# Kernel optimization log

Measured on AMD Instinct MI355X. Metric: run time of the kernel, lower is better.

## Reference

```python
import jax, jax.numpy as jnp
import numpy as np

H = 16
D_MODEL = 1024
D_K = D_MODEL // H
L = 4096


def setup_inputs() -> dict:
    key = jax.random.key(0)
    ks = jax.random.split(key, 11)
    s = 1.0 / np.sqrt(D_MODEL)
    inp = {
        "query": jax.random.normal(ks[0], (L, D_MODEL), dtype=jnp.float32),
        "key": jax.random.normal(ks[1], (L, D_MODEL), dtype=jnp.float32),
        "value": jax.random.normal(ks[2], (L, D_MODEL), dtype=jnp.float32),
        "Wq": jax.random.uniform(ks[3], (D_MODEL, D_MODEL), jnp.float32, -s, s),
        "Wk": jax.random.uniform(ks[4], (D_MODEL, D_MODEL), jnp.float32, -s, s),
        "Wv": jax.random.uniform(ks[5], (D_MODEL, D_MODEL), jnp.float32, -s, s),
        "Wo": jax.random.uniform(ks[6], (D_MODEL, D_MODEL), jnp.float32, -s, s),
        "bq": jax.random.uniform(ks[7], (D_MODEL,), jnp.float32, -s, s),
        "bk": jax.random.uniform(ks[8], (D_MODEL,), jnp.float32, -s, s),
        "bv": jax.random.uniform(ks[9], (D_MODEL,), jnp.float32, -s, s),
        "bo": jax.random.uniform(ks[10], (D_MODEL,), jnp.float32, -s, s),
    }
    return inp


def reference(query, key, value, Wq, Wk, Wv, Wo, bq, bk, bv, bo):
    # projections: torch Linear computes x @ W.T + b
    def proj(x, W, b):
        # [L, d_model] -> [h, L, d_k]
        y = x @ W.T + b
        return y.reshape(L, H, D_K).transpose(1, 0, 2)

    q = proj(query, Wq, bq)   # [h, L, d_k]
    k = proj(key, Wk, bk)
    v = proj(value, Wv, bv)

    scores = jnp.einsum("hqd,hkd->hqk", q, k) / jnp.sqrt(jnp.float32(D_K))  # [h, L, L]
    p = jax.nn.softmax(scores, axis=-1)
    x = jnp.einsum("hqk,hkd->hqd", p, v)         # [h, L, d_k]
    x = x.transpose(1, 0, 2).reshape(L, H * D_K)  # [L, d_model]
    return x @ Wo.T + bo
```

## Files before the change

### kernel.cpp

```cpp
#include <hip/hip_runtime.h>

#define L_SEQ 4096
#define DM 1024
#define NH 16
#define DK 64

typedef short s16x8 __attribute__((ext_vector_type(8)));
typedef float f32x4 __attribute__((ext_vector_type(4)));
typedef float f32x8 __attribute__((ext_vector_type(8)));
typedef float f32x16 __attribute__((ext_vector_type(16)));
typedef unsigned short u16t;
typedef unsigned int u32t;

typedef __attribute__((address_space(1))) unsigned int as1_u32;
typedef __attribute__((address_space(3))) unsigned int as3_u32;

#define GLOAD_LDS16(gsrc, ldst) \
  __builtin_amdgcn_global_load_lds((as1_u32*)(gsrc), (as3_u32*)(ldst), 16, 0, 0)

__device__ __forceinline__ u16t f2bf(float f) {
  union { float f; unsigned u; } v; v.f = f;
  unsigned u = v.u;
  u += 0x7fffu + ((u >> 16) & 1u);
  return (u16t)(u >> 16);
}

__device__ __forceinline__ float fexp2(float x) {
  float r;
  asm("v_exp_f32 %0, %1" : "=v"(r) : "v"(x));
  return r;
}

__device__ __forceinline__ float bflo(u32t u) {
  union { u32t u; float f; } v; v.u = u << 16; return v.f;
}
__device__ __forceinline__ float bfhi(u32t u) {
  union { u32t u; float f; } v; v.u = u & 0xffff0000u; return v.f;
}

struct CvtArgs { const float* s[7]; u16t* d[7]; };

__global__ __launch_bounds__(256) void cvt_all(CvtArgs a) {
  int g = blockIdx.x * 256 + threadIdx.x;
  int seg, off;
  if (g < 1572864) { seg = g >> 19;               off = g & 524287; }
  else             { int t = g - 1572864; seg = 3 + (t >> 17); off = t & 131071; }
  const float* src = a.s[seg] + (size_t)off * 8;
  u16t* dst = a.d[seg] + (size_t)off * 8;
  float4 x = *(const float4*)(src);
  float4 y = *(const float4*)(src + 4);
  uint4 o;
  o.x = (u32t)f2bf(x.x) | ((u32t)f2bf(x.y) << 16);
  o.y = (u32t)f2bf(x.z) | ((u32t)f2bf(x.w) << 16);
  o.z = (u32t)f2bf(y.x) | ((u32t)f2bf(y.y) << 16);
  o.w = (u32t)f2bf(y.z) | ((u32t)f2bf(y.w) << 16);
  *(uint4*)dst = o;
}

struct QkvArgs {
  const u16t* A[3]; const u16t* Bm[3]; const float* bias[3]; u16t* C[3];
  float scale0;
};

__global__ __launch_bounds__(256)
void gemm_qkv(QkvArgs ga) {
  __shared__ unsigned char lds[2][2][8192];
  const int flat = blockIdx.x;
  const int bid = (flat & 7) * 96 + (flat >> 3);
  const int z = bid >> 8;
  const int b = bid & 255;
  const int bc = (z == 2) ? (b & 31) : (b & 7);
  const int br = (z == 2) ? (b >> 5) : (b >> 3);
  const int N  = (z == 2) ? L_SEQ : DM;
  const float osc = (z == 0) ? ga.scale0 : 1.0f;
  const bool rowb = (z == 2);
  const u16t* A = ga.A[z];
  const u16t* Bm = ga.Bm[z];
  const float* bias = ga.bias[z];
  u16t* C = ga.C[z];
  const int K = DM;

  const int tid = threadIdx.x;
  const int lane = tid & 63;
  const int wv = tid >> 6;
  const int wr = wv >> 1, wc = wv & 1;
  const int l15 = lane & 15, l4 = lane >> 4;

  const int r_st = tid >> 2;
  const int c_st = (tid & 3) ^ ((r_st >> 1) & 3);
  const u16t* a0 = A + (size_t)(br * 128 + r_st) * K + c_st * 8;
  const u16t* a1 = a0 + (size_t)64 * K;
  const u16t* b0 = Bm + (size_t)(bc * 128 + r_st) * K + c_st * 8;
  const u16t* b1 = b0 + (size_t)64 * K;
  const int woff = wv * 1024;

  f32x4 acc[4][4] = {};

  auto stage = [&](int buf, int k0) {
    GLOAD_LDS16(a0 + k0, &lds[buf][0][woff]);
    GLOAD_LDS16(a1 + k0, &lds[buf][0][4096 + woff]);
    GLOAD_LDS16(b0 + k0, &lds[buf][1][woff]);
    GLOAD_LDS16(b1 + k0, &lds[buf][1][4096 + woff]);
  };

  const int nt = K >> 5;
  stage(0, 0);
  int buf = 0;
  for (int t = 0; t < nt; ++t) {
    __syncthreads();
    if (t + 1 < nt) stage(buf ^ 1, (t + 1) * 32);
    s16x8 af[4], bfr[4];
    #pragma unroll
    for (int m = 0; m < 4; ++m) {
      int r = wr * 64 + m * 16 + l15;
      int sl = l4 ^ ((r >> 1) & 3);
      af[m] = *(const s16x8*)&lds[buf][0][r * 64 + (sl << 4)];
    }
    #pragma unroll
    for (int n = 0; n < 4; ++n) {
      int r = wc * 64 + n * 16 + l15;
      int sl = l4 ^ ((r >> 1) & 3);
      bfr[n] = *(const s16x8*)&lds[buf][1][r * 64 + (sl << 4)];
    }
    #pragma unroll
    for (int m = 0; m < 4; ++m)
      #pragma unroll
      for (int n = 0; n < 4; ++n)
        acc[m][n] = __builtin_amdgcn_mfma_f32_16x16x32_bf16(af[m], bfr[n], acc[m][n], 0, 0, 0);
    buf ^= 1;
  }

  const int l15p = rowb ? ((l15 & 3) | ((l15 & 4) << 1) | ((l15 & 8) >> 1)) : l15;

  #pragma unroll
  for (int m = 0; m < 4; ++m) {
    #pragma unroll
    for (int n = 0; n < 4; ++n) {
      #pragma unroll
      for (int i = 0; i < 4; ++i) {
        int row = br * 128 + wr * 64 + m * 16 + l4 * 4 + i;
        int col = bc * 128 + wc * 64 + n * 16 + l15p;
        float v = (acc[m][n][i] + (rowb ? bias[row] : bias[col])) * osc;
        C[(size_t)row * N + col] = f2bf(v);
      }
    }
  }
}

__global__ __launch_bounds__(256)
void gemm_out(const u16t* __restrict__ A, const u16t* __restrict__ B,
              const float* __restrict__ bias, float* __restrict__ C,
              int M, int N, int K) {
  __shared__ unsigned char lds[2][12288];
  const int tid = threadIdx.x;
  const int lane = tid & 63;
  const int wv = tid >> 6;
  const int wr = wv >> 1, wc = wv & 1;
  const int l15 = lane & 15, l4 = lane >> 4;
  const int flat = blockIdx.x + (blockIdx.y << 4);
  const int nsw = (flat & 7) * 64 + (flat >> 3);
  const int bc = nsw & 15, br = nsw >> 4;

  const int r_st = tid >> 2;
  const int c_st = (tid & 3) ^ ((r_st >> 1) & 3);
  const u16t* a0 = A + (size_t)(br * 128 + r_st) * K + c_st * 8;
  const u16t* a1 = a0 + (size_t)64 * K;
  const u16t* b0 = B + (size_t)(bc * 64 + r_st) * K + c_st * 8;
  const int woff = wv * 1024;

  f32x4 acc[4][2] = {};

  auto stage = [&](int buf, int k0) {
    GLOAD_LDS16(a0 + k0, &lds[buf][woff]);
    GLOAD_LDS16(a1 + k0, &lds[buf][4096 + woff]);
    GLOAD_LDS16(b0 + k0, &lds[buf][8192 + woff]);
  };

  const int nt = K >> 5;
  stage(0, 0);
  int buf = 0;
  for (int t = 0; t < nt; ++t) {
    __syncthreads();
    if (t + 1 < nt) stage(buf ^ 1, (t + 1) * 32);
    s16x8 af[4], bfr[2];
    #pragma unroll
    for (int m = 0; m < 4; ++m) {
      int r = wr * 64 + m * 16 + l15;
      int sl = l4 ^ ((r >> 1) & 3);
      af[m] = *(const s16x8*)&lds[buf][r * 64 + (sl << 4)];
    }
    #pragma unroll
    for (int n = 0; n < 2; ++n) {
      int r = wc * 32 + n * 16 + l15;
      int sl = l4 ^ ((r >> 1) & 3);
      bfr[n] = *(const s16x8*)&lds[buf][8192 + r * 64 + (sl << 4)];
    }
    #pragma unroll
    for (int m = 0; m < 4; ++m)
      #pragma unroll
      for (int n = 0; n < 2; ++n)
        acc[m][n] = __builtin_amdgcn_mfma_f32_16x16x32_bf16(af[m], bfr[n], acc[m][n], 0, 0, 0);
    buf ^= 1;
  }

  #pragma unroll
  for (int m = 0; m < 4; ++m) {
    #pragma unroll
    for (int n = 0; n < 2; ++n) {
      #pragma unroll
      for (int i = 0; i < 4; ++i) {
        int row = br * 128 + wr * 64 + m * 16 + l4 * 4 + i;
        int col = bc * 64 + wc * 32 + n * 16 + l15;
        C[(size_t)row * N + col] = acc[m][n][i] + bias[col];
      }
    }
  }
}

#define PKBF(dst, a, b) \
  asm("v_cvt_pk_bf16_f32 %0, %1, %2" : "=v"(dst) : "v"(a), "v"(b))

#define MAKE_FRAG(S, B, FR) { \
    union { u32t u[4]; s16x8 v; } uu; \
    PKBF(uu.u[0], S[B + 0], S[B + 1]); \
    PKBF(uu.u[1], S[B + 2], S[B + 3]); \
    PKBF(uu.u[2], S[B + 4], S[B + 5]); \
    PKBF(uu.u[3], S[B + 6], S[B + 7]); \
    FR = uu.v; }

__global__ __launch_bounds__(512, 4)
void attn_fused(const u16t* __restrict__ Qp, const u16t* __restrict__ Kp,
                const u16t* __restrict__ VpT, u16t* __restrict__ Op,
                float* __restrict__ Ml) {
  __shared__ unsigned char sStage[3][16384];

  const int tid = threadIdx.x;
  const int lane = tid & 63;
  const int w = tid >> 6;
  const int l31 = lane & 31;
  const int hi = lane >> 5;
  const int flat = blockIdx.x;
  const int nsw = (flat & 7) * 64 + (flat >> 3);
  const int qt = nsw & 15;
  const int h = (nsw >> 4) & 15;
  const int z = nsw >> 8;
  const int kvbase = z * (L_SEQ / 2);
  const int qrow = qt * 256 + w * 32 + l31;
  u16t* Opz = Op + (size_t)z * (L_SEQ * DM);
  float* Mlz = Ml + z * (NH * L_SEQ);

  s16x8 qf[4];
  {
    const u16t* qsrc = Qp + (size_t)qrow * DM + h * DK + hi * 8;
    #pragma unroll
    for (int c = 0; c < 4; ++c) qf[c] = *(const s16x8*)(qsrc + c * 16);
  }

  f32x16 acc0 = {}, acc1 = {};
  float lrow = 0.f;

  const u16t* kptr = Kp + (size_t)(kvbase + lane) * DM + h * DK + w * 8;
  const u16t* vptr = VpT + (size_t)(h * DK + lane) * L_SEQ + kvbase + w * 8;
  const int woffK = w * 1024;

  auto stage = [&](int buf) {
    GLOAD_LDS16(kptr, &sStage[buf][woffK]);
    GLOAD_LDS16(vptr, &sStage[buf][8192 + woffK]);
    kptr += 64 * DM;
    vptr += 64;
  };

  const int rdoff = (hi << 10) + (l31 << 4);

  auto compute = [&](const unsigned char* sb) {
    f32x16 st0 = {}, st1 = {};
    __builtin_amdgcn_s_setprio(1);
    #pragma unroll
    for (int c = 0; c < 4; ++c) {
      s16x8 kf0 = *(const s16x8*)(sb + c * 2048);
      s16x8 kf1 = *(const s16x8*)(sb + c * 2048 + 512);
      st0 = __builtin_amdgcn_mfma_f32_32x32x16_bf16(kf0, qf[c], st0, 0, 0, 0);
      st1 = __builtin_amdgcn_mfma_f32_32x32x16_bf16(kf1, qf[c], st1, 0, 0, 0);
    }
    __builtin_amdgcn_s_setprio(0);

    #pragma unroll
    for (int r = 0; r < 16; ++r) {
      st0[r] = fexp2(st0[r]);
      st1[r] = fexp2(st1[r]);
    }
    f32x16 sv = st0 + st1;
    f32x8 s8v = __builtin_shufflevector(sv, sv, 0, 1, 2, 3, 4, 5, 6, 7) +
                __builtin_shufflevector(sv, sv, 8, 9, 10, 11, 12, 13, 14, 15);
    f32x4 s4v = __builtin_shufflevector(s8v, s8v, 0, 1, 2, 3) +
                __builtin_shufflevector(s8v, s8v, 4, 5, 6, 7);
    lrow += (s4v[0] + s4v[1]) + (s4v[2] + s4v[3]);

    __builtin_amdgcn_s_setprio(1);
    #pragma unroll
    for (int cc = 0; cc < 4; ++cc) {
      s16x8 pfr;
      if (cc == 0)      MAKE_FRAG(st0, 0, pfr)
      else if (cc == 1) MAKE_FRAG(st0, 8, pfr)
      else if (cc == 2) MAKE_FRAG(st1, 0, pfr)
      else              MAKE_FRAG(st1, 8, pfr)
      s16x8 vf0 = *(const s16x8*)(sb + 8192 + cc * 2048);
      s16x8 vf1 = *(const s16x8*)(sb + 8192 + cc * 2048 + 512);
      acc0 = __builtin_amdgcn_mfma_f32_32x32x16_bf16(vf0, pfr, acc0, 0, 0, 0);
      acc1 = __builtin_amdgcn_mfma_f32_32x32x16_bf16(vf1, pfr, acc1, 0, 0, 0);
    }
    __builtin_amdgcn_s_setprio(0);
  };

  auto phase = [&](int bc, int bs) {
    asm volatile("s_waitcnt vmcnt(2)" ::: "memory");
    __builtin_amdgcn_s_barrier();
    __builtin_amdgcn_sched_barrier(0);
    stage(bs);
    compute(sStage[bc] + rdoff);
  };

  stage(0);
  stage(1);
  #pragma unroll 1
  for (int c = 0; c < 10; ++c) {
    phase(0, 2);
    phase(1, 0);
    phase(2, 1);
  }
  asm volatile("s_waitcnt vmcnt(2)" ::: "memory");
  __builtin_amdgcn_s_barrier();
  __builtin_amdgcn_sched_barrier(0);
  compute(sStage[0] + rdoff);
  asm volatile("s_waitcnt vmcnt(0)" ::: "memory");
  __builtin_amdgcn_s_barrier();
  __builtin_amdgcn_sched_barrier(0);
  compute(sStage[1] + rdoff);

  lrow += __shfl_xor(lrow, 32);
  u16t* orow = Opz + (size_t)qrow * DM + h * DK;
  #pragma unroll
  for (int rq = 0; rq < 4; ++rq) {
    union { u16t h4[4]; uint2 v; } p0, p1;
    #pragma unroll
    for (int i = 0; i < 4; ++i) {
      p0.h4[i] = f2bf(acc0[4 * rq + i]);
      p1.h4[i] = f2bf(acc1[4 * rq + i]);
    }
    int d0 = 8 * rq + 4 * hi;
    *(uint2*)(orow + d0)      = p0.v;
    *(uint2*)(orow + 32 + d0) = p1.v;
  }
  if (hi == 0) Mlz[h * L_SEQ + qrow] = lrow;
}

__global__ __launch_bounds__(256)
void attn_combine(const u16t* __restrict__ Op, const float* __restrict__ Ml,
                  u16t* __restrict__ AO) {
  int g = blockIdx.x * 256 + threadIdx.x;
  int qh = g >> 2;
  int d0 = (g & 3) * 16;
  int q = qh >> 4, h = qh & 15;
  size_t off = (size_t)q * DM + h * DK + d0;
  const size_t OSTR = (size_t)L_SEQ * DM;

  int mi = h * L_SEQ + q;
  float inv = 1.0f / (Ml[mi] + Ml[NH * L_SEQ + mi]);

  uint4 a[2], b[2], o[2];
  a[0] = *(const uint4*)(Op + off);         a[1] = *(const uint4*)(Op + off + 8);
  b[0] = *(const uint4*)(Op + OSTR + off);  b[1] = *(const uint4*)(Op + OSTR + off + 8);
  #pragma unroll
  for (int k = 0; k < 2; ++k) {
    u32t* au = (u32t*)&a[k]; u32t* bu = (u32t*)&b[k]; u32t* ou = (u32t*)&o[k];
    #pragma unroll
    for (int j = 0; j < 4; ++j) {
      float lo = (bflo(au[j]) + bflo(bu[j])) * inv;
      float hf = (bfhi(au[j]) + bfhi(bu[j])) * inv;
      ou[j] = (u32t)f2bf(lo) | ((u32t)f2bf(hf) << 16);
    }
  }
  *(uint4*)(AO + off)     = o[0];
  *(uint4*)(AO + off + 8) = o[1];
}

extern "C" void kernel_launch(void* const* d_in, const int* in_sizes, int n_in,
                              void* d_out, int out_size, void* d_ws, size_t ws_size,
                              hipStream_t stream) {
  const float* query = (const float*)d_in[0];
  const float* key_  = (const float*)d_in[1];
  const float* value = (const float*)d_in[2];
  const float* Wq = (const float*)d_in[3];
  const float* Wk = (const float*)d_in[4];
  const float* Wv = (const float*)d_in[5];
  const float* Wo = (const float*)d_in[6];
  const float* bq = (const float*)d_in[7];
  const float* bk = (const float*)d_in[8];
  const float* bv = (const float*)d_in[9];
  const float* bo = (const float*)d_in[10];

  char* ws = (char*)d_ws;
  const size_t MB = 1u << 20;
  u16t* qb  = (u16t*)(ws + 0 * MB);
  u16t* kb  = (u16t*)(ws + 8 * MB);
  u16t* vb  = (u16t*)(ws + 16 * MB);
  u16t* wqb = (u16t*)(ws + 24 * MB);
  u16t* wkb = (u16t*)(ws + 26 * MB);
  u16t* wvb = (u16t*)(ws + 28 * MB);
  u16t* wob = (u16t*)(ws + 30 * MB);
  u16t* Qp  = (u16t*)(ws + 32 * MB);
  u16t* Kp  = (u16t*)(ws + 40 * MB);
  u16t* VpT = (u16t*)(ws + 48 * MB);
  u16t* AO  = (u16t*)(ws + 56 * MB);

  u16t* Op  = (u16t*)(ws + 0 * MB);
  float* Ml = (float*)(ws + 16 * MB);

  const float QSCALE = 0.125f * 1.4426950408889634f;

  CvtArgs ca;
  ca.s[0] = query; ca.s[1] = key_; ca.s[2] = value;
  ca.s[3] = Wq; ca.s[4] = Wk; ca.s[5] = Wv; ca.s[6] = Wo;
  ca.d[0] = qb; ca.d[1] = kb; ca.d[2] = vb;
  ca.d[3] = wqb; ca.d[4] = wkb; ca.d[5] = wvb; ca.d[6] = wob;
  cvt_all<<<dim3(8192), dim3(256), 0, stream>>>(ca);

  QkvArgs ga;
  ga.A[0] = qb;  ga.Bm[0] = wqb; ga.bias[0] = bq; ga.C[0] = Qp;
  ga.A[1] = kb;  ga.Bm[1] = wkb; ga.bias[1] = bk; ga.C[1] = Kp;
  ga.A[2] = wvb; ga.Bm[2] = vb;  ga.bias[2] = bv; ga.C[2] = VpT;
  ga.scale0 = QSCALE;
  gemm_qkv<<<dim3(768), dim3(256), 0, stream>>>(ga);

  attn_fused<<<dim3(512), dim3(512), 0, stream>>>(Qp, Kp, VpT, Op, Ml);

  attn_combine<<<dim3(1024), dim3(256), 0, stream>>>(Op, Ml, AO);

  gemm_out<<<dim3(DM / 64, L_SEQ / 128), dim3(256), 0, stream>>>(
      AO, wob, bo, (float*)d_out, L_SEQ, DM, DM);
}
```

Baseline: 149.0 us.

## Triple-buffer LDS staging in QKV and output projection GEMMs

Replaces the double-buffered global-to-LDS pipeline in both projection GEMMs with a three-stage ring buffer. Loads run two tiles ahead, and partial vmcnt waits replace full __syncthreads drains. The loop count is hardcoded to 32 K-tiles, so K must equal 1024. The aim is to hide more global-load latency behind MFMA work, at the cost of more LDS per block, which may lower occupancy.

```diff
diff --git a/kernel.cpp b/kernel.cpp
--- a/kernel.cpp
+++ b/kernel.cpp
@@ -64,7 +64,7 @@
 
 __global__ __launch_bounds__(256)
 void gemm_qkv(QkvArgs ga) {
-  __shared__ unsigned char lds[2][2][8192];
+  __shared__ unsigned char lds[3][16384];
   const int flat = blockIdx.x;
   const int bid = (flat & 7) * 96 + (flat >> 3);
   const int z = bid >> 8;
@@ -97,38 +97,56 @@
   f32x4 acc[4][4] = {};
 
   auto stage = [&](int buf, int k0) {
-    GLOAD_LDS16(a0 + k0, &lds[buf][0][woff]);
-    GLOAD_LDS16(a1 + k0, &lds[buf][0][4096 + woff]);
-    GLOAD_LDS16(b0 + k0, &lds[buf][1][woff]);
-    GLOAD_LDS16(b1 + k0, &lds[buf][1][4096 + woff]);
-  };
-
-  const int nt = K >> 5;
-  stage(0, 0);
-  int buf = 0;
-  for (int t = 0; t < nt; ++t) {
-    __syncthreads();
-    if (t + 1 < nt) stage(buf ^ 1, (t + 1) * 32);
+    GLOAD_LDS16(a0 + k0, &lds[buf][woff]);
+    GLOAD_LDS16(a1 + k0, &lds[buf][4096 + woff]);
+    GLOAD_LDS16(b0 + k0, &lds[buf][8192 + woff]);
+    GLOAD_LDS16(b1 + k0, &lds[buf][12288 + woff]);
+  };
+
+  auto compute = [&](int buf) {
     s16x8 af[4], bfr[4];
     #pragma unroll
     for (int m = 0; m < 4; ++m) {
       int r = wr * 64 + m * 16 + l15;
       int sl = l4 ^ ((r >> 1) & 3);
-      af[m] = *(const s16x8*)&lds[buf][0][r * 64 + (sl << 4)];
+      af[m] = *(const s16x8*)&lds[buf][r * 64 + (sl << 4)];
     }
     #pragma unroll
     for (int n = 0; n < 4; ++n) {
       int r = wc * 64 + n * 16 + l15;
       int sl = l4 ^ ((r >> 1) & 3);
-      bfr[n] = *(const s16x8*)&lds[buf][1][r * 64 + (sl << 4)];
+      bfr[n] = *(const s16x8*)&lds[buf][8192 + r * 64 + (sl << 4)];
     }
     #pragma unroll
     for (int m = 0; m < 4; ++m)
       #pragma unroll
       for (int n = 0; n < 4; ++n)
         acc[m][n] = __builtin_amdgcn_mfma_f32_16x16x32_bf16(af[m], bfr[n], acc[m][n], 0, 0, 0);
-    buf ^= 1;
-  }
+  };
+
+  stage(0, 0);
+  stage(1, 32);
+  int t = 0;
+  #pragma unroll 1
+  for (int c = 0; c < 10; ++c) {
+    #pragma unroll
+    for (int ph = 0; ph < 3; ++ph) {
+      asm volatile("s_waitcnt vmcnt(4)" ::: "memory");
+      __builtin_amdgcn_s_barrier();
+      __builtin_amdgcn_sched_barrier(0);
+      stage((t + 2) % 3, (t + 2) * 32);
+      compute(t % 3);
+      ++t;
+    }
+  }
+  asm volatile("s_waitcnt vmcnt(4)" ::: "memory");
+  __builtin_amdgcn_s_barrier();
+  __builtin_amdgcn_sched_barrier(0);
+  compute(0);
+  asm volatile("s_waitcnt vmcnt(0)" ::: "memory");
+  __builtin_amdgcn_s_barrier();
+  __builtin_amdgcn_sched_barrier(0);
+  compute(1);
 
   const int l15p = rowb ? ((l15 & 3) | ((l15 & 4) << 1) | ((l15 & 8) >> 1)) : l15;
 
@@ -151,7 +169,7 @@
 void gemm_out(const u16t* __restrict__ A, const u16t* __restrict__ B,
               const float* __restrict__ bias, float* __restrict__ C,
               int M, int N, int K) {
-  __shared__ unsigned char lds[2][12288];
+  __shared__ unsigned char lds[3][12288];
   const int tid = threadIdx.x;
   const int lane = tid & 63;
   const int wv = tid >> 6;
@@ -176,12 +194,7 @@
     GLOAD_LDS16(b0 + k0, &lds[buf][8192 + woff]);
   };
 
-  const int nt = K >> 5;
-  stage(0, 0);
-  int buf = 0;
-  for (int t = 0; t < nt; ++t) {
-    __syncthreads();
-    if (t + 1 < nt) stage(buf ^ 1, (t + 1) * 32);
+  auto compute = [&](int buf) {
     s16x8 af[4], bfr[2];
     #pragma unroll
     for (int m = 0; m < 4; ++m) {
@@ -200,8 +213,31 @@
       #pragma unroll
       for (int n = 0; n < 2; ++n)
         acc[m][n] = __builtin_amdgcn_mfma_f32_16x16x32_bf16(af[m], bfr[n], acc[m][n], 0, 0, 0);
-    buf ^= 1;
-  }
+  };
+
+  stage(0, 0);
+  stage(1, 32);
+  int t = 0;
+  #pragma unroll 1
+  for (int c = 0; c < 10; ++c) {
+    #pragma unroll
+    for (int ph = 0; ph < 3; ++ph) {
+      asm volatile("s_waitcnt vmcnt(3)" ::: "memory");
+      __builtin_amdgcn_s_barrier();
+      __builtin_amdgcn_sched_barrier(0);
+      stage((t + 2) % 3, (t + 2) * 32);
+      compute(t % 3);
+      ++t;
+    }
+  }
+  asm volatile("s_waitcnt vmcnt(3)" ::: "memory");
+  __builtin_amdgcn_s_barrier();
+  __builtin_amdgcn_sched_barrier(0);
+  compute(0);
+  asm volatile("s_waitcnt vmcnt(0)" ::: "memory");
+  __builtin_amdgcn_s_barrier();
+  __builtin_amdgcn_sched_barrier(0);
+  compute(1);
 
   #pragma unroll
   for (int m = 0; m < 4; ++m) {
```

Result: faster. 144.8 us, median of 3 (-2.8%).
